# Kernel optimization log

Hardware: AMD Instinct MI355X
Metric: run time of the kernel (lower is better)

## Reference

```python
import jax, jax.numpy as jnp
import numpy as np

BS, CAMS, NQ, EMBED = 1, 6, 6400, 256
HEADS, LEVELS, POINTS, DEPTH = 8, 4, 8, 4
DH = EMBED // HEADS
SHAPES = np.array([[64, 176], [32, 88], [16, 44], [8, 22]], dtype=np.int64)  # (H, W) per level
FLEN = int((SHAPES[:, 0] * SHAPES[:, 1]).sum())  # 14960


def setup_inputs() -> dict:
    key = jax.random.key(0)
    ks = jax.random.split(key, 12)
    s = 0.02
    lsi = np.concatenate([[0], np.cumsum(SHAPES[:, 0] * SHAPES[:, 1])[:-1]]).astype(np.int64)
    return {
        'query': jax.random.normal(ks[0], (BS, NQ, EMBED), jnp.float32),
        'key': jax.random.normal(ks[1], (BS, FLEN, CAMS, EMBED), jnp.float32),
        'value': jax.random.normal(ks[2], (BS, FLEN, CAMS, EMBED), jnp.float32),
        'query_pos': jax.random.normal(ks[3], (BS, NQ, EMBED), jnp.float32),
        'reference_points_cam': jax.random.uniform(ks[4], (CAMS, BS, NQ, DEPTH, 2), jnp.float32),
        'bev_mask': jax.random.bernoulli(ks[5], 0.1, (CAMS, BS, NQ, DEPTH)),
        'spatial_shapes': jnp.asarray(SHAPES),
        'level_start_index': jnp.asarray(lsi),
        'Wv': jax.random.normal(ks[6], (EMBED, EMBED), jnp.float32) * s,
        'bv': jnp.zeros((EMBED,), jnp.float32),
        'Wso': jax.random.normal(ks[7], (EMBED, HEADS * LEVELS * POINTS * 2), jnp.float32) * s,
        'bso': jax.random.normal(ks[8], (HEADS * LEVELS * POINTS * 2,), jnp.float32) * s,
        'Waw': jax.random.normal(ks[9], (EMBED, HEADS * LEVELS * POINTS), jnp.float32) * s,
        'baw': jnp.zeros((HEADS * LEVELS * POINTS,), jnp.float32),
        'Wout': jax.random.normal(ks[10], (EMBED, EMBED), jnp.float32) * s,
        'bout': jnp.zeros((EMBED,), jnp.float32),
    }


def _bilinear_gather(v, xi, yi, Wl, Hl):
    # v: (B, Hl*Wl, H, Dh); xi, yi: (B, Nq, H, P) integer-valued floats.
    # grid_sample(padding_mode='zeros'): out-of-range corners contribute 0.
    valid = (xi >= 0) & (xi < Wl) & (yi >= 0) & (yi < Hl)
    idx = (jnp.clip(yi, 0, Hl - 1) * Wl + jnp.clip(xi, 0, Wl - 1)).astype(jnp.int32)
    B, Nq, Hh, P = idx.shape
    idx2 = idx.transpose(0, 1, 3, 2).reshape(B, Nq * P, Hh)[..., None]
    g = jnp.take_along_axis(v, idx2, axis=1)  # (B, Nq*P, Hh, Dh)
    g = g.reshape(B, Nq, P, Hh, -1).transpose(0, 1, 3, 2, 4)  # (B, Nq, Hh, P, Dh)
    return jnp.where(valid[..., None], g, 0.0)


def _msda(v, loc, aw):
    # Multi-scale deformable attn: v (B, Len, H, Dh); loc in [0,1] (B, Nq, H, L, P, 2); aw (B, Nq, H, L, P).
    out = 0.0
    start = 0
    for l in range(LEVELS):
        Hl, Wl = int(SHAPES[l, 0]), int(SHAPES[l, 1])
        vl = v[:, start:start + Hl * Wl]
        start += Hl * Wl
        # align_corners=False pixel coords
        x = loc[:, :, :, l, :, 0] * Wl - 0.5
        y = loc[:, :, :, l, :, 1] * Hl - 0.5
        x0 = jnp.floor(x)
        y0 = jnp.floor(y)
        wx1 = x - x0
        wy1 = y - y0
        s = (_bilinear_gather(vl, x0, y0, Wl, Hl) * ((1 - wx1) * (1 - wy1))[..., None]
             + _bilinear_gather(vl, x0 + 1, y0, Wl, Hl) * (wx1 * (1 - wy1))[..., None]
             + _bilinear_gather(vl, x0, y0 + 1, Wl, Hl) * ((1 - wx1) * wy1)[..., None]
             + _bilinear_gather(vl, x0 + 1, y0 + 1, Wl, Hl) * (wx1 * wy1)[..., None])
        out = out + jnp.einsum('bqhpd,bqhp->bqhd', s, aw[:, :, :, l])
    B, Nq = out.shape[0], out.shape[1]
    return out.reshape(B, Nq, -1)


def reference(query, key, value, query_pos, reference_points_cam, bev_mask,
              spatial_shapes, level_start_index, Wv, bv, Wso, bso, Waw, baw, Wout, bout):
    bs, nq, C = query.shape
    cams = bev_mask.shape[0]
    inp_residual = query  # residual is taken BEFORE query_pos is added
    q = query + query_pos
    # per-camera query visibility from batch-0 mask (as in the torch loop over bev_mask)
    mask_q = jnp.any(bev_mask[:, 0], axis=-1)  # (cams, nq)
    # instead of gather-rebatch to max_len, run attention for all queries and mask the scatter-add
    q_cam = jnp.broadcast_to(q[:, None], (bs, cams, nq, C)).reshape(bs * cams, nq, C)
    ref = jnp.transpose(reference_points_cam, (1, 0, 2, 3, 4)).reshape(bs * cams, nq, DEPTH, 2)
    v = jnp.transpose(value, (2, 0, 1, 3)).reshape(bs * cams, -1, C)
    # MSDeformableAttention3D (BEVFormer): value_proj, offsets, softmax weights, bilinear sampling
    v = (v @ Wv + bv).reshape(bs * cams, -1, HEADS, DH)
    off = (q_cam @ Wso + bso).reshape(bs * cams, nq, HEADS, LEVELS, POINTS, 2)
    norm = jnp.stack([spatial_shapes[:, 1], spatial_shapes[:, 0]], -1).astype(off.dtype)  # (L, 2) = (W, H)
    off = off / norm[None, None, None, :, None, :]
    aw = jax.nn.softmax((q_cam @ Waw + baw).reshape(bs * cams, nq, HEADS, LEVELS * POINTS), axis=-1)
    aw = aw.reshape(bs * cams, nq, HEADS, LEVELS, POINTS)
    pa = POINTS // DEPTH  # xy points per Z anchor
    loc = ref[:, :, None, None, None, :, :] + off.reshape(bs * cams, nq, HEADS, LEVELS, pa, DEPTH, 2)
    loc = loc.reshape(bs * cams, nq, HEADS, LEVELS, POINTS, 2)
    out = _msda(v, loc, aw).reshape(bs, cams, nq, C)
    # scatter-add back: slots[b, q] += sum_cam visible(cam, q) * out[b, cam, q]
    slots = jnp.sum(out * mask_q[None, :, :, None].astype(out.dtype), axis=1)
    count = jnp.any(bev_mask, axis=-1).transpose(1, 2, 0).sum(-1).astype(slots.dtype)  # (bs, nq)
    count = jnp.maximum(count, 1.0)
    slots = slots / count[..., None]
    slots = slots @ Wout + bout
    return slots + inp_residual  # dropout in eval mode = identity
```

## Files before the change

kernel.cpp:

```cpp
#include <hip/hip_runtime.h>
#include <hip/hip_bf16.h>

#define CAMS   6
#define NQ     6400
#define EMBED  256
#define HEADS  8
#define LEVELS 4
#define POINTS 8
#define DEPTH  4
#define DH     32
#define FLEN   14960
#define MV     (FLEN * CAMS)
#define NCHUNK 2805

__constant__ int c_LW[4] = {176, 88, 44, 22};
__constant__ int c_LH[4] = {64, 32, 16, 8};
__constant__ int c_LS[4] = {0, 11264, 14080, 14784};

typedef __bf16 bf16x8 __attribute__((ext_vector_type(8)));
typedef float  f32x4  __attribute__((ext_vector_type(4)));

__device__ __forceinline__ ushort f2bf(float x) {
    __hip_bfloat16 h = __float2bfloat16(x);
    return *(ushort*)&h;
}
__device__ __forceinline__ float bflo(unsigned u) { return __uint_as_float(u << 16); }
__device__ __forceinline__ float bfhi(unsigned u) { return __uint_as_float(u & 0xffff0000u); }

__device__ __forceinline__ bf16x8 pack8(float4 a, float4 b) {
    union { ushort u[8]; bf16x8 v; } r;
    r.u[0] = f2bf(a.x); r.u[1] = f2bf(a.y); r.u[2] = f2bf(a.z); r.u[3] = f2bf(a.w);
    r.u[4] = f2bf(b.x); r.u[5] = f2bf(b.y); r.u[6] = f2bf(b.z); r.u[7] = f2bf(b.w);
    return r.v;
}

#define LSTRIDE 40

template <int MODE>
__device__ __forceinline__ void gemm_body(ushort* sA, ushort* sB,
                                          const float* __restrict__ A,
                                          const float* __restrict__ A2,
                                          const float* __restrict__ W, int ldw,
                                          const float* __restrict__ bias,
                                          const float* __restrict__ resid,
                                          float* __restrict__ Cout, int ldc, int M,
                                          int bx, int by) {
    const int t = threadIdx.x;
    const int wave = t >> 6;
    const int lane = t & 63;
    const int wm = wave & 1, wn = wave >> 1;
    const int lane15 = lane & 15;
    const int laneq = lane >> 4;
    const int row0 = bx * 128;
    const int col0 = by * 128;

    f32x4 acc[4][4] = {};

    const int a_m = t >> 3;
    const int a_k = (t & 7) * 4;
    const int b_n = t & 127;
    const int b_k = (t >> 7) * 4;

    float4 aR[4], wR[4];

    #pragma unroll
    for (int p = 0; p < 4; ++p) {
        int gm = row0 + a_m + p * 32;
        if (gm >= M) gm = M - 1;
        aR[p] = *(const float4*)(A + (size_t)gm * 256 + a_k);
    }
    #pragma unroll
    for (int p = 0; p < 4; ++p) {
        const int k = b_k + p * 8;
        const float* wp = W + (size_t)k * ldw + col0 + b_n;
        wR[p] = make_float4(wp[0], wp[ldw], wp[2 * ldw], wp[3 * ldw]);
    }

    for (int k0 = 0; k0 < 256; k0 += 32) {
        #pragma unroll
        for (int p = 0; p < 4; ++p) {
            const int m = a_m + p * 32;
            float4 a4 = aR[p];
            if (MODE == 1) {
                int gm = row0 + m;
                if (gm >= M) gm = M - 1;
                float4 b4 = *(const float4*)(A2 + (size_t)gm * 256 + k0 + a_k);
                a4.x += b4.x; a4.y += b4.y; a4.z += b4.z; a4.w += b4.w;
            }
            *(ushort4*)(&sA[m * LSTRIDE + a_k]) =
                make_ushort4(f2bf(a4.x), f2bf(a4.y), f2bf(a4.z), f2bf(a4.w));
        }
        #pragma unroll
        for (int p = 0; p < 4; ++p) {
            const int k = b_k + p * 8;
            *(ushort4*)(&sB[b_n * LSTRIDE + k]) =
                make_ushort4(f2bf(wR[p].x), f2bf(wR[p].y), f2bf(wR[p].z), f2bf(wR[p].w));
        }
        __syncthreads();

        if (k0 + 32 < 256) {
            #pragma unroll
            for (int p = 0; p < 4; ++p) {
                int gm = row0 + a_m + p * 32;
                if (gm >= M) gm = M - 1;
                aR[p] = *(const float4*)(A + (size_t)gm * 256 + k0 + 32 + a_k);
            }
            #pragma unroll
            for (int p = 0; p < 4; ++p) {
                const int k = b_k + p * 8;
                const float* wp = W + (size_t)(k0 + 32 + k) * ldw + col0 + b_n;
                wR[p] = make_float4(wp[0], wp[ldw], wp[2 * ldw], wp[3 * ldw]);
            }
        }

        bf16x8 af[4], bfr[4];
        #pragma unroll
        for (int i = 0; i < 4; ++i) {
            const int m = wm * 64 + i * 16 + lane15;
            af[i] = *(const bf16x8*)(&sA[m * LSTRIDE + laneq * 8]);
            const int n = wn * 64 + i * 16 + lane15;
            bfr[i] = *(const bf16x8*)(&sB[n * LSTRIDE + laneq * 8]);
        }
        #pragma unroll
        for (int i = 0; i < 4; ++i)
            #pragma unroll
            for (int j = 0; j < 4; ++j)
                acc[i][j] = __builtin_amdgcn_mfma_f32_16x16x32_bf16(af[i], bfr[j], acc[i][j], 0, 0, 0);
        __syncthreads();
    }

    #pragma unroll
    for (int j = 0; j < 4; ++j) {
        const int col = col0 + wn * 64 + j * 16 + lane15;
        const float bcol = bias[col];
        #pragma unroll
        for (int i = 0; i < 4; ++i) {
            #pragma unroll
            for (int r = 0; r < 4; ++r) {
                const int row = row0 + wm * 64 + i * 16 + laneq * 4 + r;
                if (row < M) {
                    float v = acc[i][j][r] + bcol;
                    if (MODE == 3) v += resid[(size_t)row * 256 + col];
                    Cout[(size_t)row * ldc + col] = v;
                }
            }
        }
    }
}

__device__ __forceinline__ void vproj_body(ushort* sW,
                                           const float* __restrict__ A,
                                           const float* __restrict__ W,
                                           const float* __restrict__ bias,
                                           ushort* __restrict__ v_ws,
                                           int bid) {
    const int t = threadIdx.x;

    {
        const int n = t;
        const int xr = (n & 7) << 3;
        #pragma unroll 8
        for (int r = 0; r < 64; ++r) {
            const int k4 = r * 4;
            const float w0 = W[(size_t)(k4 + 0) * 256 + n];
            const float w1 = W[(size_t)(k4 + 1) * 256 + n];
            const float w2 = W[(size_t)(k4 + 2) * 256 + n];
            const float w3 = W[(size_t)(k4 + 3) * 256 + n];
            *(ushort4*)(&sW[n * 256 + (k4 ^ xr)]) =
                make_ushort4(f2bf(w0), f2bf(w1), f2bf(w2), f2bf(w3));
        }
    }
    __syncthreads();

    const int wave = t >> 6, lane = t & 63;
    const int lane15 = lane & 15, laneq = lane >> 4;

    float bcol[16];
    #pragma unroll
    for (int nt = 0; nt < 16; ++nt) bcol[nt] = bias[nt * 16 + lane15];

    const int g = bid * 4 + wave;
    for (int c = g; c < NCHUNK; c += 1024) {
        const int rowbase = c * 32;
        const float* ap0 = A + (size_t)(rowbase + lane15) * 256 + laneq * 8;
        const float* ap1 = ap0 + 16 * 256;

        float4 a[2][8][2];
        #pragma unroll
        for (int s = 0; s < 8; ++s) {
            a[0][s][0] = *(const float4*)(ap0 + s * 32);
            a[0][s][1] = *(const float4*)(ap0 + s * 32 + 4);
            a[1][s][0] = *(const float4*)(ap1 + s * 32);
            a[1][s][1] = *(const float4*)(ap1 + s * 32 + 4);
        }

        f32x4 acc[2][16] = {};
        #pragma unroll
        for (int s = 0; s < 8; ++s) {
            const bf16x8 fa0 = pack8(a[0][s][0], a[0][s][1]);
            const bf16x8 fa1 = pack8(a[1][s][0], a[1][s][1]);
            const int kb = laneq * 8 + s * 32;
            #pragma unroll
            for (int nt = 0; nt < 16; ++nt) {
                const int n = nt * 16 + lane15;
                const bf16x8 fb = *(const bf16x8*)(&sW[n * 256 + (kb ^ ((n & 7) << 3))]);
                acc[0][nt] = __builtin_amdgcn_mfma_f32_16x16x32_bf16(fa0, fb, acc[0][nt], 0, 0, 0);
                acc[1][nt] = __builtin_amdgcn_mfma_f32_16x16x32_bf16(fa1, fb, acc[1][nt], 0, 0, 0);
            }
        }

        #pragma unroll
        for (int rt = 0; rt < 2; ++rt) {
            #pragma unroll
            for (int r = 0; r < 4; ++r) {
                const int row = rowbase + rt * 16 + laneq * 4 + r;
                const unsigned pix = ((unsigned)row * 43691u) >> 18;
                const unsigned cam = (unsigned)row - pix * 6u;
                const unsigned base = (cam * 8u * FLEN + pix) * 32u;
                #pragma unroll
                for (int nt = 0; nt < 16; ++nt) {
                    const unsigned idx = base + (unsigned)(nt >> 1) * (FLEN * 32u)
                                       + (unsigned)((nt & 1) * 16 + lane15);
                    v_ws[idx] = f2bf(acc[rt][nt][r] + bcol[nt]);
                }
            }
        }
    }
}

__launch_bounds__(256, 1)
__global__ void fused_pre_gemm(const float* __restrict__ value,
                               const float* __restrict__ query,
                               const float* __restrict__ query_pos,
                               const float* __restrict__ Wv,  const float* __restrict__ bv,
                               const float* __restrict__ Wso, const float* __restrict__ bso,
                               const float* __restrict__ Waw, const float* __restrict__ baw,
                               const void* __restrict__ bm,
                               ushort* __restrict__ v_ws,
                               float* __restrict__ off_ws,
                               float* __restrict__ aw_ws,
                               int* __restrict__ flag) {
    __shared__ ushort sW[256 * 256];
    const int bid = blockIdx.x;
    if (bid < 256) {
        vproj_body(sW, value, Wv, bv, v_ws, bid);
    } else if (bid < 456) {
        const int r = bid - 256;
        gemm_body<1>(sW, sW + 128 * LSTRIDE, query, query_pos, Wso, 512, bso, nullptr,
                     off_ws, 512, NQ, r >> 2, r & 3);
    } else if (bid < 556) {
        const int r = bid - 456;
        gemm_body<1>(sW, sW + 128 * LSTRIDE, query, query_pos, Waw, 256, baw, nullptr,
                     aw_ws, 256, NQ, r >> 1, r & 1);
    } else {
        const int t = threadIdx.x;
        const uint4* p4 = (const uint4*)bm;
        unsigned acc = 0;
        for (int i = t; i < (CAMS * NQ * DEPTH) / 16; i += 256) {
            const uint4 w = p4[i];
            acc |= w.x | w.y | w.z | w.w;
        }
        #pragma unroll
        for (int off = 32; off >= 1; off >>= 1) acc |= __shfl_xor(acc, off);
        unsigned* sred = (unsigned*)sW;
        if ((t & 63) == 0) sred[t >> 6] = acc;
        __syncthreads();
        if (t == 0) {
            const unsigned a = sred[0] | sred[1] | sred[2] | sred[3];
            flag[0] = (a & 0xFFFFFF00u) ? 1 : 0;
        }
    }
}

__launch_bounds__(256)
__global__ void gemm_out_kernel(const float* __restrict__ slots,
                                const float* __restrict__ Wout,
                                const float* __restrict__ bout,
                                const float* __restrict__ query,
                                float* __restrict__ out) {
    __shared__ ushort sA[128 * LSTRIDE];
    __shared__ ushort sB[128 * LSTRIDE];
    const int bid = blockIdx.x;
    gemm_body<3>(sA, sB, slots, nullptr, Wout, 256, bout, query,
                 out, 256, NQ, bid >> 1, bid & 1);
}

__launch_bounds__(256)
__global__ void sample_kernel(const ushort* __restrict__ v,
                              const float* __restrict__ off_ws,
                              const float* __restrict__ aw_logit,
                              const float* __restrict__ rp,
                              const void* __restrict__ bm,
                              const int* __restrict__ flag,
                              float* __restrict__ slots) {
    const int q = blockIdx.x;
    const int t = threadIdx.x;
    const int h = t >> 5;
    const int e8 = (t >> 2) & 7;
    const int ch8 = (t & 3) * 8;
    const int l = e8 >> 1;
    const int ebase = h * 32 + e8 * 4;

    const int Wl = c_LW[l], Hl = c_LH[l], St = c_LS[l];
    const float fWl = (float)Wl, fHl = (float)Hl;

    const int fmt = *flag;
    int am = 0, cnt = 0;
    if (fmt == 1) {
        #pragma unroll
        for (int cam = 0; cam < CAMS; ++cam) {
            const unsigned w = ((const unsigned*)bm)[cam * NQ + q];
            const int a = (w != 0u);
            am |= a << cam;
            cnt += a;
        }
    } else {
        #pragma unroll
        for (int cam = 0; cam < CAMS; ++cam) {
            const int4 w = ((const int4*)bm)[cam * NQ + q];
            const int a = ((w.x | w.y | w.z | w.w) != 0);
            am |= a << cam;
            cnt += a;
        }
    }
    const float invq = 1.0f / (float)(cnt > 0 ? cnt : 1);

    const float4 lg = *(const float4*)(aw_logit + (size_t)q * 256 + ebase);
    float mx = fmaxf(fmaxf(lg.x, lg.y), fmaxf(lg.z, lg.w));
    mx = fmaxf(mx, __shfl_xor(mx, 4));
    mx = fmaxf(mx, __shfl_xor(mx, 8));
    mx = fmaxf(mx, __shfl_xor(mx, 16));
    const float e0 = expf(lg.x - mx), e1 = expf(lg.y - mx);
    const float e2 = expf(lg.z - mx), e3 = expf(lg.w - mx);
    float s = e0 + e1 + e2 + e3;
    s += __shfl_xor(s, 4);
    s += __shfl_xor(s, 8);
    s += __shfl_xor(s, 16);
    const float sc = invq / s;
    const float awv[4] = {e0 * sc, e1 * sc, e2 * sc, e3 * sc};

    const float* ofp = off_ws + (size_t)q * 512 + ebase * 2;
    const float4 o01 = *(const float4*)(ofp);
    const float4 o23 = *(const float4*)(ofp + 4);
    const float offx[4] = {o01.x, o01.z, o23.x, o23.z};
    const float offy[4] = {o01.y, o01.w, o23.y, o23.w};

    float acc[8] = {};

    for (int cam = 0; cam < CAMS; ++cam) {
        if (!((am >> cam) & 1)) continue;

        const int camhF = (cam * 8 + h) * FLEN + St;

        const float4 r01 = *(const float4*)(rp + (size_t)cam * (NQ * 8) + q * 8);
        const float4 r23 = *(const float4*)(rp + (size_t)cam * (NQ * 8) + q * 8 + 4);
        const float rx[4] = {r01.x, r01.z, r23.x, r23.z};
        const float ry[4] = {r01.y, r01.w, r23.y, r23.w};

        int   addr[16];
        float wgt[16];
        #pragma unroll
        for (int j = 0; j < 4; ++j) {
            const float x = fmaf(rx[j], fWl, offx[j]) - 0.5f;
            const float y = fmaf(ry[j], fHl, offy[j]) - 0.5f;
            const float x0f = floorf(x), y0f = floorf(y);
            const int x0 = (int)x0f, y0 = (int)y0f;
            const float fx = x - x0f, fy = y - y0f;
            const float wx0 = 1.f - fx, wy0 = 1.f - fy;
            #pragma unroll
            for (int c = 0; c < 4; ++c) {
                const int cx = x0 + (c & 1);
                const int cy = y0 + (c >> 1);
                const bool valid = ((unsigned)cx < (unsigned)Wl) & ((unsigned)cy < (unsigned)Hl);
                const int pixo = valid ? (cy * Wl + cx) : 0;
                addr[j * 4 + c] = ((camhF + pixo) << 5) + ch8;
                wgt[j * 4 + c] = valid
                    ? (((c & 1) ? fx : wx0) * ((c >> 1) ? fy : wy0) * awv[j])
                    : 0.f;
            }
        }
        #pragma unroll
        for (int i = 0; i < 16; ++i) {
            const uint4 u = *(const uint4*)(v + addr[i]);
            const float w = wgt[i];
            acc[0] = fmaf(w, bflo(u.x), acc[0]);
            acc[1] = fmaf(w, bfhi(u.x), acc[1]);
            acc[2] = fmaf(w, bflo(u.y), acc[2]);
            acc[3] = fmaf(w, bfhi(u.y), acc[3]);
            acc[4] = fmaf(w, bflo(u.z), acc[4]);
            acc[5] = fmaf(w, bfhi(u.z), acc[5]);
            acc[6] = fmaf(w, bflo(u.w), acc[6]);
            acc[7] = fmaf(w, bfhi(u.w), acc[7]);
        }
    }

    #pragma unroll
    for (int i = 0; i < 8; ++i) {
        acc[i] += __shfl_xor(acc[i], 4);
        acc[i] += __shfl_xor(acc[i], 8);
        acc[i] += __shfl_xor(acc[i], 16);
    }
    slots[(size_t)q * 256 + h * 32 + ch8 + e8] = acc[e8];
}

extern "C" void kernel_launch(void* const* d_in, const int* in_sizes, int n_in,
                              void* d_out, int out_size, void* d_ws, size_t ws_size,
                              hipStream_t stream) {
    const float* query     = (const float*)d_in[0];
    const float* value     = (const float*)d_in[2];
    const float* query_pos = (const float*)d_in[3];
    const float* refpts    = (const float*)d_in[4];
    const void*  bev_mask  = d_in[5];
    const float* Wv   = (const float*)d_in[8];
    const float* bv   = (const float*)d_in[9];
    const float* Wso  = (const float*)d_in[10];
    const float* bso  = (const float*)d_in[11];
    const float* Waw  = (const float*)d_in[12];
    const float* baw  = (const float*)d_in[13];
    const float* Wout = (const float*)d_in[14];
    const float* bout = (const float*)d_in[15];
    float* out = (float*)d_out;

    ushort* v_ws  = (ushort*)d_ws;
    float* off_ws = (float*)(v_ws + (size_t)MV * 256);
    float* aw_ws  = off_ws + (size_t)NQ * 512;
    float* slots  = aw_ws + (size_t)NQ * 256;
    int*   flag   = (int*)(slots + (size_t)NQ * 256);

    hipLaunchKernelGGL(fused_pre_gemm, dim3(557), dim3(256), 0, stream,
                       value, query, query_pos, Wv, bv, Wso, bso, Waw, baw,
                       bev_mask, v_ws, off_ws, aw_ws, flag);

    hipLaunchKernelGGL(sample_kernel, dim3(NQ), dim3(256), 0, stream,
                       v_ws, off_ws, aw_ws, refpts, bev_mask, flag, slots);

    hipLaunchKernelGGL(gemm_out_kernel, dim3(100), dim3(256), 0, stream,
                       slots, Wout, bout, query, out);
}
```

Before: 355.9 us.

## Unify pre-GEMMs as weight-stationary blocks and double-buffer camera gathers in sampler

The small query projections (offsets, attention weights) now reuse the weight-stationary MFMA body that the value projection uses, with a query+pos add mode. This cuts the fused pre-GEMM grid from 557 to 257 blocks and rebalances work so value projection gets 211 blocks and each query GEMM slice gets 15. The sampling kernel software-pipelines across visible cameras, issuing the next camera's 16 gathers before it consumes the current one, so memory latency can be hidden. The cost is a large jump in register use from the doubled address, weight and data arrays, and fewer blocks for the value projection.

```diff
diff --git a/kernel.cpp b/kernel.cpp
--- a/kernel.cpp
+++ b/kernel.cpp
@@ -12,6 +12,7 @@
 #define FLEN   14960
 #define MV     (FLEN * CAMS)
 #define NCHUNK 2805
+#define NQCHUNK 200
 
 __constant__ int c_LW[4] = {176, 88, 44, 22};
 __constant__ int c_LH[4] = {64, 32, 16, 8};
@@ -36,15 +37,13 @@
 
 #define LSTRIDE 40
 
-template <int MODE>
-__device__ __forceinline__ void gemm_body(ushort* sA, ushort* sB,
-                                          const float* __restrict__ A,
-                                          const float* __restrict__ A2,
-                                          const float* __restrict__ W, int ldw,
-                                          const float* __restrict__ bias,
-                                          const float* __restrict__ resid,
-                                          float* __restrict__ Cout, int ldc, int M,
-                                          int bx, int by) {
+__device__ __forceinline__ void gemm_body_out(ushort* sA, ushort* sB,
+                                              const float* __restrict__ A,
+                                              const float* __restrict__ W, int ldw,
+                                              const float* __restrict__ bias,
+                                              const float* __restrict__ resid,
+                                              float* __restrict__ Cout, int ldc, int M,
+                                              int bx, int by) {
     const int t = threadIdx.x;
     const int wave = t >> 6;
     const int lane = t & 63;
@@ -80,13 +79,7 @@
         #pragma unroll
         for (int p = 0; p < 4; ++p) {
             const int m = a_m + p * 32;
-            float4 a4 = aR[p];
-            if (MODE == 1) {
-                int gm = row0 + m;
-                if (gm >= M) gm = M - 1;
-                float4 b4 = *(const float4*)(A2 + (size_t)gm * 256 + k0 + a_k);
-                a4.x += b4.x; a4.y += b4.y; a4.z += b4.z; a4.w += b4.w;
-            }
+            const float4 a4 = aR[p];
             *(ushort4*)(&sA[m * LSTRIDE + a_k]) =
                 make_ushort4(f2bf(a4.x), f2bf(a4.y), f2bf(a4.z), f2bf(a4.w));
         }
@@ -139,8 +132,7 @@
             for (int r = 0; r < 4; ++r) {
                 const int row = row0 + wm * 64 + i * 16 + laneq * 4 + r;
                 if (row < M) {
-                    float v = acc[i][j][r] + bcol;
-                    if (MODE == 3) v += resid[(size_t)row * 256 + col];
+                    float v = acc[i][j][r] + bcol + resid[(size_t)row * 256 + col];
                     Cout[(size_t)row * ldc + col] = v;
                 }
             }
@@ -148,12 +140,18 @@
     }
 }
 
-__device__ __forceinline__ void vproj_body(ushort* sW,
+__device__ __forceinline__ void add4(float4& a, float4 b) {
+    a.x += b.x; a.y += b.y; a.z += b.z; a.w += b.w;
+}
+
+template <int QMODE>
+__device__ __forceinline__ void wstat_body(ushort* sW,
                                            const float* __restrict__ A,
-                                           const float* __restrict__ W,
+                                           const float* __restrict__ A2,
+                                           const float* __restrict__ W, int ldw, int c0,
                                            const float* __restrict__ bias,
-                                           ushort* __restrict__ v_ws,
-                                           int bid) {
+                                           void* __restrict__ out, int ldc,
+                                           int nchunk, int blk, int nblk) {
     const int t = threadIdx.x;
 
     {
@@ -162,10 +160,10 @@
         #pragma unroll 8
         for (int r = 0; r < 64; ++r) {
             const int k4 = r * 4;
-            const float w0 = W[(size_t)(k4 + 0) * 256 + n];
-            const float w1 = W[(size_t)(k4 + 1) * 256 + n];
-            const float w2 = W[(size_t)(k4 + 2) * 256 + n];
-            const float w3 = W[(size_t)(k4 + 3) * 256 + n];
+            const float w0 = W[(size_t)(k4 + 0) * ldw + c0 + n];
+            const float w1 = W[(size_t)(k4 + 1) * ldw + c0 + n];
+            const float w2 = W[(size_t)(k4 + 2) * ldw + c0 + n];
+            const float w3 = W[(size_t)(k4 + 3) * ldw + c0 + n];
             *(ushort4*)(&sW[n * 256 + (k4 ^ xr)]) =
                 make_ushort4(f2bf(w0), f2bf(w1), f2bf(w2), f2bf(w3));
         }
@@ -177,10 +175,9 @@
 
     float bcol[16];
     #pragma unroll
-    for (int nt = 0; nt < 16; ++nt) bcol[nt] = bias[nt * 16 + lane15];
-
-    const int g = bid * 4 + wave;
-    for (int c = g; c < NCHUNK; c += 1024) {
+    for (int nt = 0; nt < 16; ++nt) bcol[nt] = bias[c0 + nt * 16 + lane15];
+
+    for (int c = blk * 4 + wave; c < nchunk; c += nblk * 4) {
         const int rowbase = c * 32;
         const float* ap0 = A + (size_t)(rowbase + lane15) * 256 + laneq * 8;
         const float* ap1 = ap0 + 16 * 256;
@@ -193,6 +190,17 @@
             a[1][s][0] = *(const float4*)(ap1 + s * 32);
             a[1][s][1] = *(const float4*)(ap1 + s * 32 + 4);
         }
+        if (QMODE == 1) {
+            const float* bp0 = A2 + (size_t)(rowbase + lane15) * 256 + laneq * 8;
+            const float* bp1 = bp0 + 16 * 256;
+            #pragma unroll
+            for (int s = 0; s < 8; ++s) {
+                add4(a[0][s][0], *(const float4*)(bp0 + s * 32));
+                add4(a[0][s][1], *(const float4*)(bp0 + s * 32 + 4));
+                add4(a[1][s][0], *(const float4*)(bp1 + s * 32));
+                add4(a[1][s][1], *(const float4*)(bp1 + s * 32 + 4));
+            }
+        }
 
         f32x4 acc[2][16] = {};
         #pragma unroll
@@ -214,14 +222,21 @@
             #pragma unroll
             for (int r = 0; r < 4; ++r) {
                 const int row = rowbase + rt * 16 + laneq * 4 + r;
-                const unsigned pix = ((unsigned)row * 43691u) >> 18;
-                const unsigned cam = (unsigned)row - pix * 6u;
-                const unsigned base = (cam * 8u * FLEN + pix) * 32u;
-                #pragma unroll
-                for (int nt = 0; nt < 16; ++nt) {
-                    const unsigned idx = base + (unsigned)(nt >> 1) * (FLEN * 32u)
-                                       + (unsigned)((nt & 1) * 16 + lane15);
-                    v_ws[idx] = f2bf(acc[rt][nt][r] + bcol[nt]);
+                if (QMODE == 0) {
+                    const unsigned pix = ((unsigned)row * 43691u) >> 18;
+                    const unsigned cam = (unsigned)row - pix * 6u;
+                    const unsigned base = (cam * 8u * FLEN + pix) * 32u;
+                    #pragma unroll
+                    for (int nt = 0; nt < 16; ++nt) {
+                        const unsigned idx = base + (unsigned)(nt >> 1) * (FLEN * 32u)
+                                           + (unsigned)((nt & 1) * 16 + lane15);
+                        ((ushort*)out)[idx] = f2bf(acc[rt][nt][r] + bcol[nt]);
+                    }
+                } else {
+                    float* op = (float*)out + (size_t)row * ldc + c0 + lane15;
+                    #pragma unroll
+                    for (int nt = 0; nt < 16; ++nt)
+                        op[nt * 16] = acc[rt][nt][r] + bcol[nt];
                 }
             }
         }
@@ -242,16 +257,14 @@
                                int* __restrict__ flag) {
     __shared__ ushort sW[256 * 256];
     const int bid = blockIdx.x;
-    if (bid < 256) {
-        vproj_body(sW, value, Wv, bv, v_ws, bid);
-    } else if (bid < 456) {
-        const int r = bid - 256;
-        gemm_body<1>(sW, sW + 128 * LSTRIDE, query, query_pos, Wso, 512, bso, nullptr,
-                     off_ws, 512, NQ, r >> 2, r & 3);
-    } else if (bid < 556) {
-        const int r = bid - 456;
-        gemm_body<1>(sW, sW + 128 * LSTRIDE, query, query_pos, Waw, 256, baw, nullptr,
-                     aw_ws, 256, NQ, r >> 1, r & 1);
+    if (bid < 211) {
+        wstat_body<0>(sW, value, nullptr, Wv, 256, 0, bv, v_ws, 0, NCHUNK, bid, 211);
+    } else if (bid < 226) {
+        wstat_body<1>(sW, query, query_pos, Wso, 512, 0,   bso, off_ws, 512, NQCHUNK, bid - 211, 15);
+    } else if (bid < 241) {
+        wstat_body<1>(sW, query, query_pos, Wso, 512, 256, bso, off_ws, 512, NQCHUNK, bid - 226, 15);
+    } else if (bid < 256) {
+        wstat_body<1>(sW, query, query_pos, Waw, 256, 0,   baw, aw_ws, 256, NQCHUNK, bid - 241, 15);
     } else {
         const int t = threadIdx.x;
         const uint4* p4 = (const uint4*)bm;
@@ -281,9 +294,55 @@
     __shared__ ushort sA[128 * LSTRIDE];
     __shared__ ushort sB[128 * LSTRIDE];
     const int bid = blockIdx.x;
-    gemm_body<3>(sA, sB, slots, nullptr, Wout, 256, bout, query,
-                 out, 256, NQ, bid >> 1, bid & 1);
-}
+    gemm_body_out(sA, sB, slots, Wout, 256, bout, query, out, 256, NQ, bid >> 1, bid & 1);
+}
+
+#define STAGE(ADDR, WGT, UU, CAM) do {                                          \
+    const int cam_ = (CAM);                                                     \
+    const float4 r01_ = *(const float4*)(rp + (size_t)cam_ * (NQ * 8) + q * 8); \
+    const float4 r23_ = *(const float4*)(rp + (size_t)cam_ * (NQ * 8) + q * 8 + 4); \
+    const float rx_[4] = {r01_.x, r01_.z, r23_.x, r23_.z};                      \
+    const float ry_[4] = {r01_.y, r01_.w, r23_.y, r23_.w};                      \
+    const int camhF_ = (cam_ * 8 + h) * FLEN + St;                              \
+    _Pragma("unroll")                                                           \
+    for (int j = 0; j < 4; ++j) {                                               \
+        const float x = fmaf(rx_[j], fWl, offx[j]) - 0.5f;                      \
+        const float y = fmaf(ry_[j], fHl, offy[j]) - 0.5f;                      \
+        const float x0f = floorf(x), y0f = floorf(y);                           \
+        const int x0 = (int)x0f, y0 = (int)y0f;                                 \
+        const float fx = x - x0f, fy = y - y0f;                                 \
+        const float wx0 = 1.f - fx, wy0 = 1.f - fy;                             \
+        _Pragma("unroll")                                                       \
+        for (int cc = 0; cc < 4; ++cc) {                                        \
+            const int cx = x0 + (cc & 1);                                       \
+            const int cy = y0 + (cc >> 1);                                      \
+            const bool valid = ((unsigned)cx < (unsigned)Wl) & ((unsigned)cy < (unsigned)Hl); \
+            const int pixo = valid ? (cy * Wl + cx) : 0;                        \
+            ADDR[j * 4 + cc] = ((camhF_ + pixo) << 5) + ch8;                    \
+            WGT[j * 4 + cc] = valid                                             \
+                ? (((cc & 1) ? fx : wx0) * ((cc >> 1) ? fy : wy0) * awv[j])     \
+                : 0.f;                                                          \
+        }                                                                       \
+    }                                                                           \
+    _Pragma("unroll")                                                           \
+    for (int i = 0; i < 16; ++i) UU[i] = *(const uint4*)(v + ADDR[i]);          \
+} while (0)
+
+#define CONSUME(UU, WGT) do {                                                   \
+    _Pragma("unroll")                                                           \
+    for (int i = 0; i < 16; ++i) {                                              \
+        const uint4 u = UU[i];                                                  \
+        const float w = WGT[i];                                                 \
+        accv[0] = fmaf(w, bflo(u.x), accv[0]);                                  \
+        accv[1] = fmaf(w, bfhi(u.x), accv[1]);                                  \
+        accv[2] = fmaf(w, bflo(u.y), accv[2]);                                  \
+        accv[3] = fmaf(w, bfhi(u.y), accv[3]);                                  \
+        accv[4] = fmaf(w, bflo(u.z), accv[4]);                                  \
+        accv[5] = fmaf(w, bfhi(u.z), accv[5]);                                  \
+        accv[6] = fmaf(w, bflo(u.w), accv[6]);                                  \
+        accv[7] = fmaf(w, bfhi(u.w), accv[7]);                                  \
+    }                                                                           \
+} while (0)
 
 __launch_bounds__(256)
 __global__ void sample_kernel(const ushort* __restrict__ v,
@@ -345,62 +404,35 @@
     const float offx[4] = {o01.x, o01.z, o23.x, o23.z};
     const float offy[4] = {o01.y, o01.w, o23.y, o23.w};
 
-    float acc[8] = {};
-
-    for (int cam = 0; cam < CAMS; ++cam) {
-        if (!((am >> cam) & 1)) continue;
-
-        const int camhF = (cam * 8 + h) * FLEN + St;
-
-        const float4 r01 = *(const float4*)(rp + (size_t)cam * (NQ * 8) + q * 8);
-        const float4 r23 = *(const float4*)(rp + (size_t)cam * (NQ * 8) + q * 8 + 4);
-        const float rx[4] = {r01.x, r01.z, r23.x, r23.z};
-        const float ry[4] = {r01.y, r01.w, r23.y, r23.w};
-
-        int   addr[16];
-        float wgt[16];
-        #pragma unroll
-        for (int j = 0; j < 4; ++j) {
-            const float x = fmaf(rx[j], fWl, offx[j]) - 0.5f;
-            const float y = fmaf(ry[j], fHl, offy[j]) - 0.5f;
-            const float x0f = floorf(x), y0f = floorf(y);
-            const int x0 = (int)x0f, y0 = (int)y0f;
-            const float fx = x - x0f, fy = y - y0f;
-            const float wx0 = 1.f - fx, wy0 = 1.f - fy;
-            #pragma unroll
-            for (int c = 0; c < 4; ++c) {
-                const int cx = x0 + (c & 1);
-                const int cy = y0 + (c >> 1);
-                const bool valid = ((unsigned)cx < (unsigned)Wl) & ((unsigned)cy < (unsigned)Hl);
-                const int pixo = valid ? (cy * Wl + cx) : 0;
-                addr[j * 4 + c] = ((camhF + pixo) << 5) + ch8;
-                wgt[j * 4 + c] = valid
-                    ? (((c & 1) ? fx : wx0) * ((c >> 1) ? fy : wy0) * awv[j])
-                    : 0.f;
-            }
-        }
-        #pragma unroll
-        for (int i = 0; i < 16; ++i) {
-            const uint4 u = *(const uint4*)(v + addr[i]);
-            const float w = wgt[i];
-            acc[0] = fmaf(w, bflo(u.x), acc[0]);
-            acc[1] = fmaf(w, bfhi(u.x), acc[1]);
-            acc[2] = fmaf(w, bflo(u.y), acc[2]);
-            acc[3] = fmaf(w, bfhi(u.y), acc[3]);
-            acc[4] = fmaf(w, bflo(u.z), acc[4]);
-            acc[5] = fmaf(w, bfhi(u.z), acc[5]);
-            acc[6] = fmaf(w, bflo(u.w), acc[6]);
-            acc[7] = fmaf(w, bfhi(u.w), acc[7]);
-        }
+    float accv[8] = {};
+
+    int   addrA[16], addrB[16];
+    float wgtA[16], wgtB[16];
+    uint4 uA[16], uB[16];
+
+    int m = am;
+    int camA = -1;
+    if (m) { camA = __ffs(m) - 1; m &= m - 1; STAGE(addrA, wgtA, uA, camA); }
+
+    #pragma unroll
+    for (int it = 0; it < 3; ++it) {
+        if (camA < 0) break;
+        int camB = -1;
+        if (m) { camB = __ffs(m) - 1; m &= m - 1; STAGE(addrB, wgtB, uB, camB); }
+        CONSUME(uA, wgtA);
+        camA = -1;
+        if (camB < 0) break;
+        if (m) { camA = __ffs(m) - 1; m &= m - 1; STAGE(addrA, wgtA, uA, camA); }
+        CONSUME(uB, wgtB);
     }
 
     #pragma unroll
     for (int i = 0; i < 8; ++i) {
-        acc[i] += __shfl_xor(acc[i], 4);
-        acc[i] += __shfl_xor(acc[i], 8);
-        acc[i] += __shfl_xor(acc[i], 16);
-    }
-    slots[(size_t)q * 256 + h * 32 + ch8 + e8] = acc[e8];
+        accv[i] += __shfl_xor(accv[i], 4);
+        accv[i] += __shfl_xor(accv[i], 8);
+        accv[i] += __shfl_xor(accv[i], 16);
+    }
+    slots[(size_t)q * 256 + h * 32 + ch8 + e8] = accv[e8];
 }
 
 extern "C" void kernel_launch(void* const* d_in, const int* in_sizes, int n_in,
@@ -427,7 +459,7 @@
     float* slots  = aw_ws + (size_t)NQ * 256;
     int*   flag   = (int*)(slots + (size_t)NQ * 256);
 
-    hipLaunchKernelGGL(fused_pre_gemm, dim3(557), dim3(256), 0, stream,
+    hipLaunchKernelGGL(fused_pre_gemm, dim3(257), dim3(256), 0, stream,
                        value, query, query_pos, Wv, bv, Wso, bso, Waw, baw,
                        bev_mask, v_ws, off_ws, aw_ws, flag);
 
```

After: 370.8 us. 4.2% more time.
